# Kernel optimization log

Hardware: AMD Instinct MI355X
Metric: run time of the kernel (lower is better)

Reference implementation:

```python
import jax, jax.numpy as jnp
import numpy as np

P = 16  # patch_size


def _tokenize(x, p):
    # (B,C,H,W) -> (B,C,nP,p,p), row-major patch order
    B, C, H, W = x.shape
    nH, nW = H // p, W // p
    x = x.reshape(B, C, nH, p, nW, p).transpose(0, 1, 2, 4, 3, 5)
    return x.reshape(B, C, nH * nW, p, p)


def _untokenize(t, p, H, W):
    B, C, nP, _, _ = t.shape
    nH, nW = H // p, W // p
    t = t.reshape(B, C, nH, nW, p, p).transpose(0, 1, 2, 4, 3, 5)
    return t.reshape(B, C, H, W)


def _sinusoidal_pe(n, d):
    pos = jnp.arange(n, dtype=jnp.float32)[:, None]                    # (n,1)
    div = jnp.exp(jnp.arange(0, d, 2, dtype=jnp.float32) * (-jnp.log(10000.0) / d))
    ang = pos * div                                                     # (n, d/2)
    pe = jnp.zeros((n, d), dtype=jnp.float32)
    pe = pe.at[:, 0::2].set(jnp.sin(ang))
    pe = pe.at[:, 1::2].set(jnp.cos(ang)[:, : d // 2])
    return pe


def setup_inputs() -> dict:
    key = jax.random.key(0)
    ks = jax.random.split(key, 7)
    B, C, H, W = 16, 3, 512, 512
    nh = 12
    D = C * P * P            # 768 token dim
    dh = D // nh             # 64 head dim
    s = 0.02
    x = jax.random.normal(ks[0], (B, C, H, W), dtype=jnp.float32)
    Wq = jax.random.normal(ks[1], (nh, D, dh), dtype=jnp.float32) * s
    Wk = jax.random.normal(ks[2], (nh, D, dh), dtype=jnp.float32) * s
    Wv = jax.random.normal(ks[3], (nh, D, dh), dtype=jnp.float32) * s
    bq = jax.random.normal(ks[4], (nh, dh), dtype=jnp.float32) * s
    bk = jax.random.normal(ks[5], (nh, dh), dtype=jnp.float32) * s
    bv = jax.random.normal(ks[6], (nh, dh), dtype=jnp.float32) * s
    return {"x": x, "Wq": Wq, "bq": bq, "Wk": Wk, "bk": bk, "Wv": Wv, "bv": bv}


def reference(x, Wq, bq, Wk, bk, Wv, bv):
    B, C, H, W = x.shape
    nh, D, dh = Wq.shape
    tok = _tokenize(x, P)                      # (B,C,nP,p,p)
    nP = tok.shape[2]
    t = tok.reshape(B, nP, D)                  # torch .view semantics (row-major reshape)
    pe = _sinusoidal_pe(nP, D)
    t = 2.0 * t + pe[None]
    # batched per-head projections (H heads, independent weights)
    q = jnp.einsum('bnd,hde->bhne', t, Wq) + bq[None, :, None, :]
    k = jnp.einsum('bnd,hde->bhne', t, Wk) + bk[None, :, None, :]
    v = jnp.einsum('bnd,hde->bhne', t, Wv) + bv[None, :, None, :]
    scores = jnp.einsum('bhne,bhme->bhnm', q, k) / jnp.sqrt(jnp.float32(dh))
    attn = jax.nn.softmax(scores, axis=-1)
    o = jnp.einsum('bhnm,bhme->bhne', attn, v)  # (B,nh,nP,dh)
    # concat heads along last dim
    out = o.transpose(0, 2, 1, 3).reshape(B, nP, D)
    out = out.reshape(B, C, nP, P, P)          # torch .view back
    return _untokenize(out, P, H, W)
```

## Files before the change

kernel.cpp:

```cpp
#include <hip/hip_runtime.h>
#include <hip/hip_bf16.h>
#include <math.h>

typedef short bf16x8 __attribute__((ext_vector_type(8)));
typedef float f32x4 __attribute__((ext_vector_type(4)));

static __device__ __forceinline__ unsigned short f2bf(float f) {
  unsigned int u = __float_as_uint(f);
  u += 0x7FFFu + ((u >> 16) & 1u);
  return (unsigned short)(u >> 16);
}

static __device__ __forceinline__ void gload16(const unsigned short* g, unsigned short* l) {
  __builtin_amdgcn_global_load_lds(
      (const __attribute__((address_space(1))) unsigned int*)g,
      (__attribute__((address_space(3))) unsigned int*)l, 16, 0, 0);
}

__global__ __launch_bounds__(256) void k_prep_w(const float* __restrict__ Wq,
                                                const float* __restrict__ Wk,
                                                const float* __restrict__ Wv,
                                                unsigned short* __restrict__ wt) {
  __shared__ unsigned short lw[64][72];
  int sh = blockIdx.x;
  int kt = blockIdx.y;
  int s = sh / 12, h = sh - s * 12;
  const float* W = (s == 0 ? Wq : (s == 1 ? Wk : Wv)) + h * 49152 + (kt << 6) * 64;
  int tid = threadIdx.x;
#pragma unroll
  for (int it = 0; it < 4; ++it) {
    int idx = it * 256 + tid;
    int kk = idx >> 4, e4 = (idx & 15) << 2;
    float4 v = *(const float4*)(W + kk * 64 + e4);
    lw[e4 + 0][kk] = f2bf(v.x);
    lw[e4 + 1][kk] = f2bf(v.y);
    lw[e4 + 2][kk] = f2bf(v.z);
    lw[e4 + 3][kk] = f2bf(v.w);
  }
  __syncthreads();
  unsigned short* outp = wt + sh * 49152 + (kt << 6);
#pragma unroll
  for (int it = 0; it < 2; ++it) {
    int c = it * 256 + tid;
    int e = c >> 3, kc = (c & 7) << 3;
    *(uint4*)(outp + e * 768 + kc) = *(const uint4*)&lw[e][kc];
  }
}

__global__ __launch_bounds__(256) void k_pe(unsigned short* __restrict__ pe) {
  int g = blockIdx.x * 256 + threadIdx.x;
  int f = g << 3;
  int m = f / 768;
  int d = f - m * 768;
  unsigned short tmp[8];
#pragma unroll
  for (int u = 0; u < 8; ++u) {
    int dd = d + u;
    int k = dd >> 1;
    float ang = (float)m * expf(-0.023985261385f * (float)k);
    tmp[u] = f2bf((dd & 1) ? cosf(ang) : sinf(ang));
  }
  *(uint4*)(pe + f) = *(const uint4*)tmp;
}

__global__ __launch_bounds__(256) void k_build_t(const float* __restrict__ x,
                                                 const unsigned short* __restrict__ pe,
                                                 unsigned short* __restrict__ t) {
  int g = blockIdx.x * 256 + threadIdx.x;
  int f = g << 3;
  int c  = f >> 18;
  int rl = f & 262143;
  int n  = rl >> 8;
  int qq = rl & 255;
  int ii = qq >> 4, jj = qq & 15;
  uint4 peu = *(const uint4*)(pe + f);
  unsigned int pw[4] = {peu.x, peu.y, peu.z, peu.w};
  float pef[8];
#pragma unroll
  for (int u = 0; u < 8; ++u)
    pef[u] = __uint_as_float(((pw[u >> 1] >> ((u & 1) * 16)) & 0xFFFFu) << 16);
  const float* xp0 = x + (c << 18) + (((n >> 5) << 4) + ii) * 512 + ((n & 31) << 4) + jj;
  for (int b = 0; b < 16; ++b) {
    const float* xp = xp0 + b * 786432;
    float4 v0 = *(const float4*)xp;
    float4 v1 = *(const float4*)(xp + 4);
    float xv[8] = {v0.x, v0.y, v0.z, v0.w, v1.x, v1.y, v1.z, v1.w};
    unsigned short tmp[8];
#pragma unroll
    for (int u = 0; u < 8; ++u) tmp[u] = f2bf(2.0f * xv[u] + pef[u]);
    *(uint4*)(t + b * 786432 + f) = *(const uint4*)tmp;
  }
}

union SMQ {
  struct { unsigned short A[2][128][32]; unsigned short B[2][128][32]; } g;
  unsigned short tr[64][136];
};
#define QKV_STEP(BUF)                                                                   \
  {                                                                                     \
    bf16x8 a[4], b[4];                                                                  \
    _Pragma("unroll") for (int mi = 0; mi < 4; ++mi)                                    \
        a[mi] = *(const bf16x8*)&sm.g.A[BUF][wm * 64 + mi * 16 + q16][g << 3];          \
    _Pragma("unroll") for (int ni = 0; ni < 4; ++ni)                                    \
        b[ni] = *(const bf16x8*)&sm.g.B[BUF][wn * 64 + ni * 16 + q16][g << 3];          \
    _Pragma("unroll") for (int mi = 0; mi < 4; ++mi)                                    \
        _Pragma("unroll") for (int ni = 0; ni < 4; ++ni)                                \
            acc[mi][ni] =                                                               \
                __builtin_amdgcn_mfma_f32_16x16x32_bf16(a[mi], b[ni], acc[mi][ni], 0, 0, 0); \
  }
__global__ __launch_bounds__(256) void k_qkv(
    const unsigned short* __restrict__ t, const unsigned short* __restrict__ wt,
    const float* __restrict__ bq, const float* __restrict__ bk, const float* __restrict__ bv,
    unsigned short* __restrict__ qout, unsigned short* __restrict__ kout,
    unsigned short* __restrict__ vout) {
  __shared__ SMQ sm;
  int bid = blockIdx.x;
  int xcd = bid & 7, idx = bid >> 3;
  int rt = xcd * 16 + idx / 18;
  int jt = idx % 18;
  int row0 = rt << 7;
  int j0 = jt << 7;
  int s = jt / 6;
  int h0 = (jt % 6) * 2;
  const float* bias = (s == 0 ? bq : (s == 1 ? bk : bv));
  unsigned short* outp = (s == 0 ? qout : (s == 1 ? kout : vout));
  int tid = threadIdx.x, lane = tid & 63, w = tid >> 6;
  int wm = w >> 1, wn = w & 1;
  int g = lane >> 4, q16 = lane & 15;
  const unsigned short* gA0 = t  + (row0 + 32 * w + (lane >> 2)) * 768 + ((lane & 3) << 3);
  const unsigned short* gA1 = gA0 + 16 * 768;
  const unsigned short* gB0 = wt + (j0 + 32 * w + (lane >> 2)) * 768 + ((lane & 3) << 3);
  const unsigned short* gB1 = gB0 + 16 * 768;
  unsigned short* lA0b0 = &sm.g.A[0][32 * w][0];
  unsigned short* lA1b0 = &sm.g.A[0][32 * w + 16][0];
  unsigned short* lB0b0 = &sm.g.B[0][32 * w][0];
  unsigned short* lB1b0 = &sm.g.B[0][32 * w + 16][0];
  unsigned short* lA0b1 = &sm.g.A[1][32 * w][0];
  unsigned short* lA1b1 = &sm.g.A[1][32 * w + 16][0];
  unsigned short* lB0b1 = &sm.g.B[1][32 * w][0];
  unsigned short* lB1b1 = &sm.g.B[1][32 * w + 16][0];
  f32x4 acc[4][4] = {};
  gload16(gA0, lA0b0); gload16(gA1, lA1b0);
  gload16(gB0, lB0b0); gload16(gB1, lB1b0);
  asm volatile("s_waitcnt vmcnt(0)" ::: "memory");
  __syncthreads();
  for (int k0 = 0; k0 < 768; k0 += 64) {
    if (k0 + 32 < 768) {
      gload16(gA0 + k0 + 32, lA0b1); gload16(gA1 + k0 + 32, lA1b1);
      gload16(gB0 + k0 + 32, lB0b1); gload16(gB1 + k0 + 32, lB1b1);
    }
    QKV_STEP(0);
    asm volatile("s_waitcnt vmcnt(0)" ::: "memory");
    __syncthreads();
    if (k0 + 64 < 768) {
      gload16(gA0 + k0 + 64, lA0b0); gload16(gA1 + k0 + 64, lA1b0);
      gload16(gB0 + k0 + 64, lB0b0); gload16(gB1 + k0 + 64, lB1b0);
    }
    QKV_STEP(1);
    asm volatile("s_waitcnt vmcnt(0)" ::: "memory");
    __syncthreads();
  }
  int bb2 = row0 >> 10, n0 = row0 & 1023;
  if (s < 2) {
    float qs = (s == 0) ? 0.18033688011f : 1.0f;
#pragma unroll
    for (int ni = 0; ni < 4; ++ni) {
      int colg = wn * 64 + ni * 16 + q16;
      int h = h0 + (colg >> 6);
      int e = colg & 63;
      float be = bias[h * 64 + e];
      int base = (bb2 * 12 + h) << 16;
#pragma unroll
      for (int mi = 0; mi < 4; ++mi)
#pragma unroll
        for (int r = 0; r < 4; ++r) {
          int n = n0 + wm * 64 + mi * 16 + (g << 2) + r;
          outp[base + (n << 6) + e] = f2bf((acc[mi][ni][r] + be) * qs);
        }
    }
  } else {
#pragma unroll
    for (int hh = 0; hh < 2; ++hh) {
      __syncthreads();
      if (wn == hh) {
#pragma unroll
        for (int ni = 0; ni < 4; ++ni) {
          int e = ni * 16 + q16;
          float be = bias[(h0 + hh) * 64 + e];
#pragma unroll
          for (int mi = 0; mi < 4; ++mi)
#pragma unroll
            for (int rp = 0; rp < 2; ++rp) {
              int rr = (wm * 2 + (mi >> 1)) * 32 + g * 8 + (mi & 1) * 4 + rp * 2;
              unsigned int lo = f2bf(acc[mi][ni][rp * 2] + be);
              unsigned int hi = f2bf(acc[mi][ni][rp * 2 + 1] + be);
              *(unsigned int*)&sm.tr[e][rr] = lo | (hi << 16);
            }
        }
      }
      __syncthreads();
      int base = (bb2 * 12 + h0 + hh) << 16;
#pragma unroll
      for (int it = 0; it < 4; ++it) {
        int c = it * 256 + tid;
        int e = c >> 4, nc = (c & 15) << 3;
        *(uint4*)(vout + base + (e << 10) + n0 + nc) = *(const uint4*)&sm.tr[e][nc];
      }
    }
  }
}

__global__ __launch_bounds__(256) void k_attn(
    const unsigned short* __restrict__ Q,
    const unsigned short* __restrict__ K,
    const unsigned short* __restrict__ Vg,
    float* __restrict__ out) {
  __shared__ unsigned short Kt[64][72];
  __shared__ unsigned short Vt[80][72];
  int bid = blockIdx.x;
  int xcd = bid & 7, idx = bid >> 3;
  int bh = xcd * 24 + (idx >> 3);
  int qt = idx & 7;
  int b = bh / 12, h = bh - b * 12;
  int tid = threadIdx.x, lane = tid & 63, w = tid >> 6;
  int g = lane >> 4, q16 = lane & 15;
  int base = bh << 16;
  const unsigned short* Qp = Q + base + (qt << 7) * 64;
  const unsigned short* Kp = K + base;
  const unsigned short* Vp = Vg + base;
  {
    int rr = 64 + (tid >> 4), c4 = (tid & 15) << 2;
    ushort4 z = {0, 0, 0, 0};
    if ((tid >> 4) == 0) { z.x = z.y = z.z = z.w = 0x3F80; }
    *(ushort4*)&Vt[rr][c4] = z;
  }
  bf16x8 qa[2][2];
#pragma unroll
  for (int mt = 0; mt < 2; ++mt)
#pragma unroll
    for (int kf = 0; kf < 2; ++kf)
      qa[mt][kf] = *(const bf16x8*)(Qp + (w * 32 + mt * 16 + q16) * 64 + kf * 32 + (g << 3));
  f32x4 o[2][5] = {};
  float mrow[2] = {-1e30f, -1e30f};
  for (int kv0 = 0; kv0 < 1024; kv0 += 64) {
    __syncthreads();
#pragma unroll
    for (int it = 0; it < 2; ++it) {
      int idx2 = it * 256 + tid;
      int rr = idx2 >> 3, cc = (idx2 & 7) << 3;
      *(uint4*)&Kt[rr][cc] = *(const uint4*)(Kp + (kv0 << 6) + (idx2 << 3));
      *(uint4*)&Vt[rr][cc] = *(const uint4*)(Vp + (rr << 10) + kv0 + cc);
    }
    __syncthreads();
    f32x4 s[2][4] = {};
#pragma unroll
    for (int cb = 0; cb < 4; ++cb) {
      bf16x8 ka0 = *(const bf16x8*)&Kt[cb * 16 + q16][g << 3];
      bf16x8 ka1 = *(const bf16x8*)&Kt[cb * 16 + q16][32 + (g << 3)];
#pragma unroll
      for (int mt = 0; mt < 2; ++mt) {
        s[mt][cb] = __builtin_amdgcn_mfma_f32_16x16x32_bf16(ka0, qa[mt][0], s[mt][cb], 0, 0, 0);
        s[mt][cb] = __builtin_amdgcn_mfma_f32_16x16x32_bf16(ka1, qa[mt][1], s[mt][cb], 0, 0, 0);
      }
    }
    float pmax[2];
#pragma unroll
    for (int mt = 0; mt < 2; ++mt) {
      float mx = s[mt][0][0];
#pragma unroll
      for (int cb = 0; cb < 4; ++cb)
#pragma unroll
        for (int r = 0; r < 4; ++r) mx = fmaxf(mx, s[mt][cb][r]);
      mx = fmaxf(mx, __shfl_xor(mx, 16));
      mx = fmaxf(mx, __shfl_xor(mx, 32));
      pmax[mt] = mx;
    }
    if (__any((pmax[0] > mrow[0] + 8.f) || (pmax[1] > mrow[1] + 8.f))) {
#pragma unroll
      for (int mt = 0; mt < 2; ++mt) {
        float mnew = fmaxf(mrow[mt], pmax[mt]);
        float sc = __builtin_amdgcn_exp2f(mrow[mt] - mnew);
        mrow[mt] = mnew;
#pragma unroll
        for (int r = 0; r < 4; ++r) {
          float scr = __shfl(sc, (g << 2) + r);
#pragma unroll
          for (int cb = 0; cb < 5; ++cb) o[mt][cb][r] *= scr;
        }
      }
    }
    unsigned int pk[2][4][2];
#pragma unroll
    for (int mt = 0; mt < 2; ++mt)
#pragma unroll
      for (int cb = 0; cb < 4; ++cb)
#pragma unroll
        for (int j2 = 0; j2 < 2; ++j2) {
          float plo = __builtin_amdgcn_exp2f(s[mt][cb][2 * j2] - mrow[mt]);
          float phi = __builtin_amdgcn_exp2f(s[mt][cb][2 * j2 + 1] - mrow[mt]);
          asm("v_cvt_pk_bf16_f32 %0, %1, %2" : "=v"(pk[mt][cb][j2]) : "v"(plo), "v"(phi));
        }
#pragma unroll
    for (int kk = 0; kk < 2; ++kk) {
      union { unsigned int u[4]; bf16x8 v; } pa[2];
#pragma unroll
      for (int mt = 0; mt < 2; ++mt) {
        pa[mt].u[0] = pk[mt][2 * kk][0];
        pa[mt].u[1] = pk[mt][2 * kk][1];
        pa[mt].u[2] = pk[mt][2 * kk + 1][0];
        pa[mt].u[3] = pk[mt][2 * kk + 1][1];
      }
#pragma unroll
      for (int cb = 0; cb < 5; ++cb) {
        bf16x8 vb = *(const bf16x8*)&Vt[cb * 16 + q16][kk * 32 + (g << 3)];
#pragma unroll
        for (int mt = 0; mt < 2; ++mt)
          o[mt][cb] = __builtin_amdgcn_mfma_f32_16x16x32_bf16(pa[mt].v, vb, o[mt][cb], 0, 0, 0);
      }
    }
  }
#pragma unroll
  for (int mt = 0; mt < 2; ++mt)
#pragma unroll
    for (int r = 0; r < 4; ++r) {
      float lr = __shfl(o[mt][4][r], lane & 48);
      float inv = 1.0f / lr;
      int m = (qt << 7) + w * 32 + mt * 16 + (g << 2) + r;
#pragma unroll
      for (int cb = 0; cb < 4; ++cb) {
        int d = (h << 6) + cb * 16 + q16;
        int f = m * 768 + d;
        int c = f >> 18, rl = f & 262143, n = rl >> 8, qq = rl & 255;
        out[((b * 3 + c) << 18) + (((n >> 5) << 4) + (qq >> 4)) * 512 + ((n & 31) << 4) + (qq & 15)] =
            o[mt][cb][r] * inv;
      }
    }
}

extern "C" void kernel_launch(void* const* d_in, const int* in_sizes, int n_in,
                              void* d_out, int out_size, void* d_ws, size_t ws_size,
                              hipStream_t stream) {
  const float* x  = (const float*)d_in[0];
  const float* Wq = (const float*)d_in[1];
  const float* bq = (const float*)d_in[2];
  const float* Wk = (const float*)d_in[3];
  const float* bk = (const float*)d_in[4];
  const float* Wv = (const float*)d_in[5];
  const float* bv = (const float*)d_in[6];
  float* out = (float*)d_out;
  unsigned short* wt = (unsigned short*)d_ws;
  unsigned short* t  = wt + 1769472;
  unsigned short* qw = t  + 12582912;
  unsigned short* kw = qw + 12582912;
  unsigned short* vw = kw + 12582912;
  unsigned short* pe = qw;
  k_pe<<<384, 256, 0, stream>>>(pe);
  k_prep_w<<<dim3(36, 12), 256, 0, stream>>>(Wq, Wk, Wv, wt);
  k_build_t<<<384, 256, 0, stream>>>(x, pe, t);
  k_qkv<<<2304, 256, 0, stream>>>(t, wt, bq, bk, bv, qw, kw, vw);
  k_attn<<<1536, 256, 0, stream>>>(qw, kw, vw, out);
}
```

Before: 204.7 us.

## Deepen QKV GEMM LDS pipeline to four stages with two loads in flight

The QKV projection GEMM moves from a double-buffered K loop that waited for all outstanding loads before each barrier to a 4-buffer ring. Two K-steps of direct global-to-LDS loads stay in flight while MFMAs run, using partial vmcnt waits and raw s_barrier plus sched_barrier. This is meant to hide global memory latency better. It doubles LDS for that kernel, which can lower occupancy, and the transpose buffer padding also changes.

```diff
diff --git a/kernel.cpp b/kernel.cpp
--- a/kernel.cpp
+++ b/kernel.cpp
@@ -93,8 +93,8 @@
 }
 
 union SMQ {
-  struct { unsigned short A[2][128][32]; unsigned short B[2][128][32]; } g;
-  unsigned short tr[64][136];
+  struct { unsigned short A[4][128][32]; unsigned short B[4][128][32]; } g;
+  unsigned short tr[64][140];
 };
 #define QKV_STEP(BUF)                                                                   \
   {                                                                                     \
@@ -108,6 +108,14 @@
             acc[mi][ni] =                                                               \
                 __builtin_amdgcn_mfma_f32_16x16x32_bf16(a[mi], b[ni], acc[mi][ni], 0, 0, 0); \
   }
+#define STAGE(KT, BUF)                                                                  \
+  gload16(gA0 + (KT) * 32, &sm.g.A[BUF][32 * w][0]);                                    \
+  gload16(gA1 + (KT) * 32, &sm.g.A[BUF][32 * w + 16][0]);                               \
+  gload16(gB0 + (KT) * 32, &sm.g.B[BUF][32 * w][0]);                                    \
+  gload16(gB1 + (KT) * 32, &sm.g.B[BUF][32 * w + 16][0]);
+#define WAITV(N) asm volatile("s_waitcnt vmcnt(" #N ")" ::: "memory")
+#define BARRIER() __builtin_amdgcn_s_barrier()
+#define SBAR() __builtin_amdgcn_sched_barrier(0)
 __global__ __launch_bounds__(256) void k_qkv(
     const unsigned short* __restrict__ t, const unsigned short* __restrict__ wt,
     const float* __restrict__ bq, const float* __restrict__ bk, const float* __restrict__ bv,
@@ -131,35 +139,20 @@
   const unsigned short* gA1 = gA0 + 16 * 768;
   const unsigned short* gB0 = wt + (j0 + 32 * w + (lane >> 2)) * 768 + ((lane & 3) << 3);
   const unsigned short* gB1 = gB0 + 16 * 768;
-  unsigned short* lA0b0 = &sm.g.A[0][32 * w][0];
-  unsigned short* lA1b0 = &sm.g.A[0][32 * w + 16][0];
-  unsigned short* lB0b0 = &sm.g.B[0][32 * w][0];
-  unsigned short* lB1b0 = &sm.g.B[0][32 * w + 16][0];
-  unsigned short* lA0b1 = &sm.g.A[1][32 * w][0];
-  unsigned short* lA1b1 = &sm.g.A[1][32 * w + 16][0];
-  unsigned short* lB0b1 = &sm.g.B[1][32 * w][0];
-  unsigned short* lB1b1 = &sm.g.B[1][32 * w + 16][0];
   f32x4 acc[4][4] = {};
-  gload16(gA0, lA0b0); gload16(gA1, lA1b0);
-  gload16(gB0, lB0b0); gload16(gB1, lB1b0);
-  asm volatile("s_waitcnt vmcnt(0)" ::: "memory");
-  __syncthreads();
-  for (int k0 = 0; k0 < 768; k0 += 64) {
-    if (k0 + 32 < 768) {
-      gload16(gA0 + k0 + 32, lA0b1); gload16(gA1 + k0 + 32, lA1b1);
-      gload16(gB0 + k0 + 32, lB0b1); gload16(gB1 + k0 + 32, lB1b1);
-    }
-    QKV_STEP(0);
-    asm volatile("s_waitcnt vmcnt(0)" ::: "memory");
-    __syncthreads();
-    if (k0 + 64 < 768) {
-      gload16(gA0 + k0 + 64, lA0b0); gload16(gA1 + k0 + 64, lA1b0);
-      gload16(gB0 + k0 + 64, lB0b0); gload16(gB1 + k0 + 64, lB1b0);
-    }
-    QKV_STEP(1);
-    asm volatile("s_waitcnt vmcnt(0)" ::: "memory");
-    __syncthreads();
-  }
+  STAGE(0, 0);
+  STAGE(1, 1);
+  for (int it = 0; it < 5; ++it) {
+    int kb = it * 4;
+    STAGE(kb + 2, 2); WAITV(8); BARRIER(); SBAR(); QKV_STEP(0);
+    STAGE(kb + 3, 3); WAITV(8); BARRIER(); SBAR(); QKV_STEP(1);
+    STAGE(kb + 4, 0); WAITV(8); BARRIER(); SBAR(); QKV_STEP(2);
+    STAGE(kb + 5, 1); WAITV(8); BARRIER(); SBAR(); QKV_STEP(3);
+  }
+  STAGE(22, 2); WAITV(8); BARRIER(); SBAR(); QKV_STEP(0);
+  STAGE(23, 3); WAITV(8); BARRIER(); SBAR(); QKV_STEP(1);
+  WAITV(4); BARRIER(); SBAR(); QKV_STEP(2);
+  WAITV(0); BARRIER(); SBAR(); QKV_STEP(3);
   int bb2 = row0 >> 10, n0 = row0 & 1023;
   if (s < 2) {
     float qs = (s == 0) ? 0.18033688011f : 1.0f;
```

Measured after the change: 194.2 us. -5.2%, faster.
